# Performance work log

Hardware: AMD Instinct MI355X
Metric: run time of the kernel (lower is better)

## Reference

```python
import jax, jax.numpy as jnp
import numpy as np

N, E = 30000, 480000
HID, NB, D = 256, 128, 2
SW = D * D * NB        # struct-encoder width = bundle_dim^2 * num_bundles = 512
NL, NSAGE = 2, 5       # outer BDL layers, SAGE layers inside struct encoder
OUT = 5
EPS = 1e-5


def _gelu(x):
    return jax.nn.gelu(x, approximate=False)  # torch nn.GELU default (exact)


def _mean_agg(x, src, dst):
    # mean over incoming edges: agg[v] = mean_{u->v} x[u]
    s = jax.ops.segment_sum(x[src], dst, num_segments=N)
    deg = jax.ops.segment_sum(jnp.ones((E,), x.dtype), dst, num_segments=N)
    return s / jnp.maximum(deg, 1.0)[:, None]


def _layernorm(x, g, b):
    m = jnp.mean(x, -1, keepdims=True)
    v = jnp.mean((x - m) ** 2, -1, keepdims=True)
    return (x - m) * jax.lax.rsqrt(v + EPS) * g + b


def _householder(X):
    # torch.nn.utils.parametrizations Orthogonal, orthogonal_map='householder':
    # Q = H_0 H_1 ... H_{d-1}, H_i = I - tau_i v_i v_i^T, v_i = strict-lower col i with unit diag
    d = X.shape[-1]
    A = jnp.tril(X, k=-1)
    tau = 2.0 / (1.0 + jnp.sum(A * A, axis=-2))  # [M, d]
    eye = jnp.eye(d, dtype=X.dtype)
    Q = jnp.broadcast_to(eye, X.shape)
    for i in range(d):
        v = A[:, :, i] + eye[i]
        Qv = jnp.einsum('mij,mj->mi', Q, v)
        Q = Q - tau[:, i, None, None] * Qv[:, :, None] * v[:, None, :]
    return Q


def _struct_encoder(h, src, dst, se_in_w, se_in_b, sage_w1, sage_b1, sage_w2, sage_b2, se_out_w, se_out_b):
    # Model('SAGE', 5, ...) with normalization='None'; dropout inactive in eval
    z = _gelu(h @ se_in_w + se_in_b)
    for i in range(NSAGE):
        m = _mean_agg(z, src, dst)
        zc = jnp.concatenate([z, m], axis=-1)  # SAGE: cat(self, mean(neigh))
        z = z + (_gelu(zc @ sage_w1[i] + sage_b1[i]) @ sage_w2[i] + sage_b2[i])
    return z @ se_out_w + se_out_b


def _forward(x, w_in, b_in, se_in_w, se_in_b, sage_w1, sage_b1, sage_w2, sage_b2,
             se_out_w, se_out_b, enc_w1, enc_b1, enc_w2, enc_b2, ln_g, ln_b,
             bdl_w1, bdl_b1, bdl_w2, bdl_b2, out_ln_g, out_ln_b, w_out, b_out, edge_index):
    src, dst = edge_index[0], edge_index[1]
    h = _gelu(x @ w_in + b_in)
    for k in range(NL):
        enc = _struct_encoder(h, src, dst, se_in_w, se_in_b, sage_w1, sage_b1,
                              sage_w2, sage_b2, se_out_w, se_out_b)
        nr = _gelu(enc @ enc_w1[k] + enc_b1[k]) @ enc_w2[k] + enc_b2[k]  # [N, SW]
        O = _householder(nr.reshape(N * NB, D, D)).reshape(N, NB, D, D)
        # BDL residual module: transport features through per-node bundle frames
        hn = _layernorm(h, ln_g[k], ln_b[k])
        hb = hn.reshape(N, NB, D)
        y = jnp.einsum('nbij,nbj->nbi', O, hb)                       # rotate into frame
        agg = _mean_agg(y.reshape(N, NB * D), src, dst).reshape(N, NB, D)
        msg = jnp.einsum('nbji,nbj->nbi', O, agg).reshape(N, NB * D)  # O^T transports back
        hc = jnp.concatenate([hn, msg], axis=-1)
        h = h + (_gelu(hc @ bdl_w1[k] + bdl_b1[k]) @ bdl_w2[k] + bdl_b2[k])
    h = _layernorm(h, out_ln_g, out_ln_b)
    return h @ w_out + b_out  # [N, OUT]; .squeeze(1) is a no-op for OUT>1


def _w(key, fan_in, shape):
    return jax.random.normal(key, shape, dtype=jnp.float32) / np.sqrt(fan_in)


def setup_inputs() -> dict:
    key = jax.random.key(0)
    ks = iter(jax.random.split(key, 40))
    f32 = jnp.float32
    return {
        'x': jax.random.normal(next(ks), (N, HID), dtype=f32),
        'edge_index': jax.random.randint(next(ks), (2, E), 0, N, dtype=jnp.int32),
        'w_in': _w(next(ks), HID, (HID, HID)), 'b_in': jnp.zeros((HID,), f32),
        'se_in_w': _w(next(ks), HID, (HID, SW)), 'se_in_b': jnp.zeros((SW,), f32),
        'sage_w1': _w(next(ks), 2 * SW, (NSAGE, 2 * SW, SW)), 'sage_b1': jnp.zeros((NSAGE, SW), f32),
        'sage_w2': _w(next(ks), SW, (NSAGE, SW, SW)), 'sage_b2': jnp.zeros((NSAGE, SW), f32),
        'se_out_w': _w(next(ks), SW, (SW, SW)), 'se_out_b': jnp.zeros((SW,), f32),
        'enc_w1': _w(next(ks), SW, (NL, SW, SW)), 'enc_b1': jnp.zeros((NL, SW), f32),
        'enc_w2': _w(next(ks), SW, (NL, SW, SW)), 'enc_b2': jnp.zeros((NL, SW), f32),
        'ln_g': jnp.ones((NL, HID), f32), 'ln_b': jnp.zeros((NL, HID), f32),
        'bdl_w1': _w(next(ks), 2 * HID, (NL, 2 * HID, HID)), 'bdl_b1': jnp.zeros((NL, HID), f32),
        'bdl_w2': _w(next(ks), HID, (NL, HID, HID)), 'bdl_b2': jnp.zeros((NL, HID), f32),
        'out_ln_g': jnp.ones((HID,), f32), 'out_ln_b': jnp.zeros((HID,), f32),
        'w_out': _w(next(ks), HID, (HID, OUT)), 'b_out': jnp.zeros((OUT,), f32),
    }


def reference(x, edge_index, w_in, b_in, se_in_w, se_in_b, sage_w1, sage_b1, sage_w2, sage_b2,
              se_out_w, se_out_b, enc_w1, enc_b1, enc_w2, enc_b2, ln_g, ln_b,
              bdl_w1, bdl_b1, bdl_w2, bdl_b2, out_ln_g, out_ln_b, w_out, b_out):
    return _forward(x, w_in, b_in, se_in_w, se_in_b, sage_w1, sage_b1, sage_w2, sage_b2,
                    se_out_w, se_out_b, enc_w1, enc_b1, enc_w2, enc_b2, ln_g, ln_b,
                    bdl_w1, bdl_b1, bdl_w2, bdl_b2, out_ln_g, out_ln_b, w_out, b_out, edge_index)
```

## Files before the change

kernel.cpp:

```cpp
#include <hip/hip_runtime.h>
#include <hip/hip_bf16.h>
#include <cstdint>
#include <cstddef>


typedef __attribute__((ext_vector_type(8))) short short8;
typedef __attribute__((ext_vector_type(4))) float f32x4;

__device__ __forceinline__ float gelu_exact(float x) {
  return 0.5f * x * (1.0f + erff(x * 0.7071067811865475f));
}
__device__ __forceinline__ unsigned short f2bf(float f) {
  __hip_bfloat16 b = __float2bfloat16(f);
  return *reinterpret_cast<unsigned short*>(&b);
}
__device__ __forceinline__ float bf2f(unsigned short u) {
  return __uint_as_float((unsigned)u << 16);
}
__device__ __forceinline__ float bflo(unsigned u) { return __uint_as_float(u << 16); }
__device__ __forceinline__ float bfhi(unsigned u) { return __uint_as_float(u & 0xffff0000u); }
__device__ __forceinline__ unsigned packbf(float f0, float f1) {
  return (unsigned)f2bf(f0) | ((unsigned)f2bf(f1) << 16);
}
__device__ __forceinline__ void gload16(const void* g, void* l) {
  __builtin_amdgcn_global_load_lds((const __attribute__((address_space(1))) void*)g,
                                   (__attribute__((address_space(3))) void*)l, 16, 0, 0);
}
#define SCHEDB() __builtin_amdgcn_sched_barrier(0)

__global__ void k_hist(const int* __restrict__ dst, int* __restrict__ deg, int E) {
  int i = blockIdx.x * 256 + threadIdx.x;
  if (i < E) atomicAdd(&deg[dst[i]], 1);
}

__global__ __launch_bounds__(1024)
void k_scan(const int* __restrict__ deg, int* __restrict__ rp, int* __restrict__ cur, int Nn) {
  __shared__ int part[1024];
  int t = threadIdx.x;
  int chunk = (Nn + 1023) >> 10;
  int s0 = t * chunk;
  int e0 = s0 + chunk; if (e0 > Nn) e0 = Nn;
  int s = 0;
  for (int i = s0; i < e0; ++i) s += deg[i];
  part[t] = s;
  __syncthreads();
  for (int off = 1; off < 1024; off <<= 1) {
    int v = (t >= off) ? part[t - off] : 0;
    __syncthreads();
    part[t] += v;
    __syncthreads();
  }
  int base = (t == 0) ? 0 : part[t - 1];
  for (int i = s0; i < e0; ++i) {
    rp[i] = base; cur[i] = base; base += deg[i];
  }
  if (t == 0) rp[Nn] = part[1023];
}

__global__ void k_fill(const int* __restrict__ src, const int* __restrict__ dst,
                       int* __restrict__ cur, int* __restrict__ srcs, int E) {
  int i = blockIdx.x * 256 + threadIdx.x;
  if (i < E) {
    int p = atomicAdd(&cur[dst[i]], 1);
    srcs[p] = src[i];
  }
}

__global__ void k_wT(const float* __restrict__ W, unsigned short* __restrict__ Wt, int K, int Nc) {
  const float* Ws = W + (size_t)blockIdx.y * K * Nc;
  unsigned short* Wd = Wt + (size_t)blockIdx.y * K * Nc;
  int idx = blockIdx.x * 256 + threadIdx.x;
  if (idx >= K * Nc) return;
  int k = idx % K, n = idx / K;
  Wd[(size_t)n * K + k] = f2bf(Ws[(size_t)k * Nc + n]);
}

__global__ void k_cast(const float* __restrict__ src, unsigned short* __restrict__ dst, int n) {
  int i = blockIdx.x * 256 + threadIdx.x;
  if (i < n) dst[i] = f2bf(src[i]);
}

template<int ACT, int RES, bool DUAL, bool W32, bool WBF, bool OP>
__global__ __launch_bounds__(256)
void k_mfma(const unsigned short* __restrict__ A1, const unsigned short* __restrict__ A2,
            int K1, int K2,
            const unsigned short* __restrict__ Wt, const float* __restrict__ bias,
            const float* R32, const unsigned short* Rbf,
            float* C32, unsigned short* Cbf, float* Op, int M, int Nc) {
  const int mb_cnt = (M + 127) >> 7;
  const int nb_cnt = Nc >> 7;
  int u = blockIdx.x;
  int xcd = u & 7;
  int rest = u >> 3;
  int nb = rest % nb_cnt;
  int mb = (rest / nb_cnt) * 8 + xcd;
  if (mb >= mb_cnt) return;
  const int m0 = mb << 7, n0 = nb << 7;

  __shared__ unsigned short As[2][128 * 64];
  __shared__ unsigned short Bs[2][128 * 64];
  const int tid = threadIdx.x;
  const int lane = tid & 63, wv = tid >> 6;
  const int wr = (wv >> 1) * 64, wc = (wv & 1) * 64;
  const int rA = lane & 15, kg = lane >> 4;
  const int Ktot = K1 + K2;
  const int nt = Ktot >> 6;

  f32x4 acc[4][4];
#pragma unroll
  for (int m = 0; m < 4; ++m)
#pragma unroll
    for (int n = 0; n < 4; ++n)
#pragma unroll
      for (int r = 0; r < 4; ++r) acc[m][n][r] = 0.f;

  auto stage = [&](int t, int b) {
    int k0 = t << 6;
    const unsigned short* Asrc; int kc, lda;
    if (!DUAL || k0 < K1) { Asrc = A1; kc = k0; lda = K1; }
    else                  { Asrc = A2; kc = k0 - K1; lda = K2; }
#pragma unroll
    for (int is = 0; is < 4; ++is) {
      int chunk = is * 256 + tid;
      int row = chunk >> 3, seg = chunk & 7;
      int ks = seg ^ (row & 7);
      int gm = m0 + row; gm = gm < M ? gm : M - 1;
      gload16(Asrc + (size_t)gm * lda + kc + ks * 8, (char*)As[b] + (size_t)chunk * 16);
      gload16(Wt + (size_t)(n0 + row) * Ktot + k0 + ks * 8, (char*)Bs[b] + (size_t)chunk * 16);
    }
  };

  stage(0, 0);
  if (nt > 1) stage(1, 1);

  for (int t = 0; t < nt; ++t) {
    const int b = t & 1;
    if (t + 1 < nt) asm volatile("s_waitcnt vmcnt(8)" ::: "memory");
    else            asm volatile("s_waitcnt vmcnt(0)" ::: "memory");
    SCHEDB();
    __builtin_amdgcn_s_barrier();
    SCHEDB();

    short8 af[2][4], bq[2][4];
#pragma unroll
    for (int kk = 0; kk < 2; ++kk) {
#pragma unroll
      for (int m = 0; m < 4; ++m) {
        int row = wr + m * 16 + rA;
        int ks = (kk * 4 + kg) ^ (row & 7);
        af[kk][m] = *reinterpret_cast<const short8*>((const char*)As[b] + row * 128 + ks * 16);
      }
#pragma unroll
      for (int n = 0; n < 4; ++n) {
        int col = wc + n * 16 + rA;
        int ks = (kk * 4 + kg) ^ (col & 7);
        bq[kk][n] = *reinterpret_cast<const short8*>((const char*)Bs[b] + col * 128 + ks * 16);
      }
    }
    asm volatile("s_waitcnt lgkmcnt(0)" ::: "memory");
    SCHEDB();
    __builtin_amdgcn_s_barrier();
    SCHEDB();
    if (t + 2 < nt) stage(t + 2, b);

    __builtin_amdgcn_s_setprio(1);
#pragma unroll
    for (int kk = 0; kk < 2; ++kk)
#pragma unroll
      for (int m = 0; m < 4; ++m)
#pragma unroll
        for (int n = 0; n < 4; ++n)
          acc[m][n] = __builtin_amdgcn_mfma_f32_16x16x32_bf16(af[kk][m], bq[kk][n],
                                                              acc[m][n], 0, 0, 0);
    __builtin_amdgcn_s_setprio(0);
  }

#pragma unroll
  for (int m = 0; m < 4; ++m) {
    int gr0 = m0 + wr + m * 16 + kg * 4;
#pragma unroll
    for (int n = 0; n < 4; ++n) {
      int gc = n0 + wc + n * 16 + rA;
      float bv = bias[gc];
#pragma unroll
      for (int r = 0; r < 4; ++r) {
        int gr = gr0 + r;
        if (gr < M) {
          float v = acc[m][n][r] + bv;
          if (ACT == 1) v = gelu_exact(v);
          if (RES == 1) v += R32[(size_t)gr * Nc + gc];
          if (RES == 2) v += bf2f(Rbf[(size_t)gr * Nc + gc]);
          if (W32) C32[(size_t)gr * Nc + gc] = v;
          if (WBF) Cbf[(size_t)gr * Nc + gc] = f2bf(v);
          if (OP) {
            if ((rA & 3) == 2) {
              float iv = 1.0f / (1.0f + v * v);
              float* op = Op + (size_t)gr * 256 + ((gc >> 2) << 1);
              op[0] = (v * v - 1.0f) * iv;
              op[1] = 2.0f * v * iv;
            }
          }
        }
      }
    }
  }
}

template<int W, bool ROT>
__global__ __launch_bounds__(256)
void k_agg(const unsigned short* __restrict__ X, const int* __restrict__ rp,
           const int* __restrict__ srcs, const float* __restrict__ o,
           unsigned short* __restrict__ out, int Nn) {
  int wid = (blockIdx.x * 256 + threadIdx.x) >> 6;
  int lane = threadIdx.x & 63;
  if (wid >= Nn) return;
  constexpr int PE = W / 64;
  float a[PE];
#pragma unroll
  for (int p = 0; p < PE; ++p) a[p] = 0.f;
  int beg = rp[wid], end = rp[wid + 1];
  for (int e = beg; e < end; ++e) {
    int s = srcs[e];
    const unsigned* row = reinterpret_cast<const unsigned*>(X + (size_t)s * W) + lane * (PE / 2);
    if (PE == 8) {
      uint4 v = *reinterpret_cast<const uint4*>(row);
      a[0] += bflo(v.x); a[1] += bfhi(v.x); a[2] += bflo(v.y); a[3] += bfhi(v.y);
      a[4] += bflo(v.z); a[5] += bfhi(v.z); a[6] += bflo(v.w); a[7] += bfhi(v.w);
    } else {
      uint2 v = *reinterpret_cast<const uint2*>(row);
      a[0] += bflo(v.x); a[1] += bfhi(v.x); a[2] += bflo(v.y); a[3] += bfhi(v.y);
    }
  }
  float inv = (end > beg) ? 1.0f / (float)(end - beg) : 0.0f;
#pragma unroll
  for (int p = 0; p < PE; ++p) a[p] *= inv;
  if (ROT) {
    float4 oc = *reinterpret_cast<const float4*>(o + (size_t)wid * 256 + lane * 4);
    float m0 = oc.x * a[0] - oc.y * a[1];
    float m1 = oc.y * a[0] + oc.x * a[1];
    float m2 = oc.z * a[2] - oc.w * a[3];
    float m3 = oc.w * a[2] + oc.z * a[3];
    a[0] = m0; a[1] = m1; a[2] = m2; a[3] = m3;
  }
  unsigned short* op = out + (size_t)wid * W + lane * PE;
  if (PE == 8) {
    uint4 rv;
    rv.x = packbf(a[0], a[1]); rv.y = packbf(a[2], a[3]);
    rv.z = packbf(a[4], a[5]); rv.w = packbf(a[6], a[7]);
    *reinterpret_cast<uint4*>(op) = rv;
  } else {
    uint2 rv;
    rv.x = packbf(a[0], a[1]); rv.y = packbf(a[2], a[3]);
    *reinterpret_cast<uint2*>(op) = rv;
  }
}

__global__ __launch_bounds__(256)
void k_ln_rot(const float* __restrict__ h, const float* __restrict__ o,
              const float* __restrict__ g, const float* __restrict__ b,
              unsigned short* __restrict__ hn, unsigned short* __restrict__ y, int Nn) {
  int wid = (blockIdx.x * 256 + threadIdx.x) >> 6;
  int lane = threadIdx.x & 63;
  if (wid >= Nn) return;
  float4 v = reinterpret_cast<const float4*>(h + (size_t)wid * 256)[lane];
  float s = v.x + v.y + v.z + v.w;
  float ss = v.x * v.x + v.y * v.y + v.z * v.z + v.w * v.w;
#pragma unroll
  for (int off = 1; off < 64; off <<= 1) { s += __shfl_xor(s, off); ss += __shfl_xor(ss, off); }
  float mean = s * (1.0f / 256.0f);
  float var = ss * (1.0f / 256.0f) - mean * mean;
  float rs = rsqrtf(var + 1e-5f);
  float4 gg = reinterpret_cast<const float4*>(g)[lane];
  float4 bb = reinterpret_cast<const float4*>(b)[lane];
  float h0 = (v.x - mean) * rs * gg.x + bb.x;
  float h1 = (v.y - mean) * rs * gg.y + bb.y;
  float h2 = (v.z - mean) * rs * gg.z + bb.z;
  float h3 = (v.w - mean) * rs * gg.w + bb.w;
  uint2 hv; hv.x = packbf(h0, h1); hv.y = packbf(h2, h3);
  *reinterpret_cast<uint2*>(hn + (size_t)wid * 256 + lane * 4) = hv;
  float4 oc = *reinterpret_cast<const float4*>(o + (size_t)wid * 256 + lane * 4);
  float y0 =  oc.x * h0 + oc.y * h1;
  float y1 = -oc.y * h0 + oc.x * h1;
  float y2 =  oc.z * h2 + oc.w * h3;
  float y3 = -oc.w * h2 + oc.z * h3;
  uint2 yv; yv.x = packbf(y0, y1); yv.y = packbf(y2, y3);
  *reinterpret_cast<uint2*>(y + (size_t)wid * 256 + lane * 4) = yv;
}

__global__ __launch_bounds__(256)
void k_final(const float* __restrict__ h, const float* __restrict__ g,
             const float* __restrict__ b, const float* __restrict__ wout,
             const float* __restrict__ bout, float* __restrict__ out, int Nn) {
  int wid = (blockIdx.x * 256 + threadIdx.x) >> 6;
  int lane = threadIdx.x & 63;
  if (wid >= Nn) return;
  float4 v = reinterpret_cast<const float4*>(h + (size_t)wid * 256)[lane];
  float s = v.x + v.y + v.z + v.w;
  float ss = v.x * v.x + v.y * v.y + v.z * v.z + v.w * v.w;
#pragma unroll
  for (int off = 1; off < 64; off <<= 1) { s += __shfl_xor(s, off); ss += __shfl_xor(ss, off); }
  float mean = s * (1.0f / 256.0f);
  float var = ss * (1.0f / 256.0f) - mean * mean;
  float rs = rsqrtf(var + 1e-5f);
  float4 gg = reinterpret_cast<const float4*>(g)[lane];
  float4 bb = reinterpret_cast<const float4*>(b)[lane];
  float hv[4];
  hv[0] = (v.x - mean) * rs * gg.x + bb.x;
  hv[1] = (v.y - mean) * rs * gg.y + bb.y;
  hv[2] = (v.z - mean) * rs * gg.z + bb.z;
  hv[3] = (v.w - mean) * rs * gg.w + bb.w;
  int c0 = lane * 4;
  float dots[5];
#pragma unroll
  for (int j = 0; j < 5; ++j) {
    float p = hv[0] * wout[(size_t)(c0 + 0) * 5 + j] + hv[1] * wout[(size_t)(c0 + 1) * 5 + j]
            + hv[2] * wout[(size_t)(c0 + 2) * 5 + j] + hv[3] * wout[(size_t)(c0 + 3) * 5 + j];
#pragma unroll
    for (int off = 1; off < 64; off <<= 1) p += __shfl_xor(p, off);
    dots[j] = p;
  }
  if (lane == 0) {
#pragma unroll
    for (int j = 0; j < 5; ++j) out[(size_t)wid * 5 + j] = dots[j] + bout[j];
  }
}

extern "C" void kernel_launch(void* const* d_in, const int* in_sizes, int n_in,
                              void* d_out, int out_size, void* d_ws, size_t ws_size,
                              hipStream_t stream) {
  const float* x       = (const float*)d_in[0];
  const int*   ei      = (const int*)  d_in[1];
  const float* w_in    = (const float*)d_in[2];
  const float* b_in    = (const float*)d_in[3];
  const float* se_in_w = (const float*)d_in[4];
  const float* se_in_b = (const float*)d_in[5];
  const float* sage_w1 = (const float*)d_in[6];
  const float* sage_b1 = (const float*)d_in[7];
  const float* sage_w2 = (const float*)d_in[8];
  const float* sage_b2 = (const float*)d_in[9];
  const float* se_out_w= (const float*)d_in[10];
  const float* se_out_b= (const float*)d_in[11];
  const float* enc_w1  = (const float*)d_in[12];
  const float* enc_b1  = (const float*)d_in[13];
  const float* enc_w2  = (const float*)d_in[14];
  const float* enc_b2  = (const float*)d_in[15];
  const float* ln_g    = (const float*)d_in[16];
  const float* ln_b    = (const float*)d_in[17];
  const float* bdl_w1  = (const float*)d_in[18];
  const float* bdl_b1  = (const float*)d_in[19];
  const float* bdl_w2  = (const float*)d_in[20];
  const float* bdl_b2  = (const float*)d_in[21];
  const float* oln_g   = (const float*)d_in[22];
  const float* oln_b   = (const float*)d_in[23];
  const float* w_out   = (const float*)d_in[24];
  const float* b_out   = (const float*)d_in[25];
  float* out = (float*)d_out;

  const int HID = 256, SW = 512;
  const int N = in_sizes[0] / HID;
  const int E = in_sizes[1] / 2;

  float* ws = (float*)d_ws;
  float* h32 = ws;
  float* o   = h32 + (size_t)N * HID;
  unsigned short* h_bf = (unsigned short*)(o + (size_t)N * HID);
  unsigned short* z_bf = h_bf + (size_t)N * HID;
  unsigned short* t_bf = z_bf + (size_t)N * SW;
  unsigned short* u_bf = t_bf + (size_t)N * SW;
  unsigned short* wts = u_bf + (size_t)N * SW;
  size_t off = 0;
  unsigned short* wt_in    = wts + off; off += 256 * 256;
  unsigned short* wt_se_in = wts + off; off += 512 * 256;
  unsigned short* wt_sage1 = wts + off; off += (size_t)5 * 512 * 1024;
  unsigned short* wt_sage2 = wts + off; off += (size_t)5 * 512 * 512;
  unsigned short* wt_se_out= wts + off; off += 512 * 512;
  unsigned short* wt_enc1  = wts + off; off += (size_t)2 * 512 * 512;
  unsigned short* wt_enc2  = wts + off; off += (size_t)2 * 512 * 512;
  unsigned short* wt_bdl1  = wts + off; off += (size_t)2 * 256 * 512;
  unsigned short* wt_bdl2  = wts + off; off += (size_t)2 * 256 * 256;
  int* deg  = (int*)(wts + off);
  int* rp   = deg + N;
  int* cur  = rp + N + 1;
  int* srcs = cur + N;
  size_t need = (size_t)((char*)(srcs + E) - (char*)d_ws);
  if (ws_size < need) return;

  unsigned short* xbf = u_bf;
  unsigned short* hn  = z_bf;
  unsigned short* y   = z_bf + (size_t)N * HID;
  unsigned short* msg = t_bf;
  unsigned short* g2  = u_bf;

  const int* esrc = ei;
  const int* edst = ei + E;

  auto cdiv = [](int a, int b) { return (a + b - 1) / b; };
  dim3 blk(256);
  int mb_cnt = cdiv(N, 128);
  int mgrp = cdiv(mb_cnt, 8);
  int g_g256 = mgrp * 8 * 2;
  int g_g512 = mgrp * 8 * 4;
  int gw = cdiv(N * 64, 256);

  hipMemsetAsync(deg, 0, sizeof(int) * N, stream);
  k_hist<<<cdiv(E, 256), blk, 0, stream>>>(edst, deg, E);
  k_scan<<<1, 1024, 0, stream>>>(deg, rp, cur, N);
  k_fill<<<cdiv(E, 256), blk, 0, stream>>>(esrc, edst, cur, srcs, E);

  auto wT = [&](const float* W, unsigned short* Wt, int K, int Nc, int cnt) {
    k_wT<<<dim3(cdiv(K * Nc, 256), cnt), blk, 0, stream>>>(W, Wt, K, Nc);
  };
  wT(w_in, wt_in, 256, 256, 1);
  wT(se_in_w, wt_se_in, 256, 512, 1);
  wT(sage_w1, wt_sage1, 1024, 512, 5);
  wT(sage_w2, wt_sage2, 512, 512, 5);
  wT(se_out_w, wt_se_out, 512, 512, 1);
  wT(enc_w1, wt_enc1, 512, 512, 2);
  wT(enc_w2, wt_enc2, 512, 512, 2);
  wT(bdl_w1, wt_bdl1, 512, 256, 2);
  wT(bdl_w2, wt_bdl2, 256, 256, 2);
  k_cast<<<cdiv(N * HID, 256), blk, 0, stream>>>(x, xbf, N * HID);

  k_mfma<1, 0, false, true, true, false><<<g_g256, blk, 0, stream>>>(
      xbf, nullptr, 256, 0, wt_in, b_in, nullptr, nullptr, h32, h_bf, nullptr, N, 256);

  for (int k = 0; k < 2; ++k) {
    k_mfma<1, 0, false, false, true, false><<<g_g512, blk, 0, stream>>>(
        h_bf, nullptr, 256, 0, wt_se_in, se_in_b, nullptr, nullptr, nullptr, z_bf, nullptr, N, 512);
    for (int i = 0; i < 5; ++i) {
      k_agg<512, false><<<gw, blk, 0, stream>>>(z_bf, rp, srcs, nullptr, t_bf, N);
      k_mfma<1, 0, true, false, true, false><<<g_g512, blk, 0, stream>>>(
          z_bf, t_bf, 512, 512, wt_sage1 + (size_t)i * 512 * 1024,
          sage_b1 + (size_t)i * SW, nullptr, nullptr, nullptr, u_bf, nullptr, N, 512);
      k_mfma<0, 2, false, false, true, false><<<g_g512, blk, 0, stream>>>(
          u_bf, nullptr, 512, 0, wt_sage2 + (size_t)i * 512 * 512,
          sage_b2 + (size_t)i * SW, nullptr, z_bf, nullptr, z_bf, nullptr, N, 512);
    }
    k_mfma<0, 0, false, false, true, false><<<g_g512, blk, 0, stream>>>(
        z_bf, nullptr, 512, 0, wt_se_out, se_out_b, nullptr, nullptr, nullptr, t_bf, nullptr, N, 512);
    k_mfma<1, 0, false, false, true, false><<<g_g512, blk, 0, stream>>>(
        t_bf, nullptr, 512, 0, wt_enc1 + (size_t)k * 512 * 512,
        enc_b1 + (size_t)k * SW, nullptr, nullptr, nullptr, u_bf, nullptr, N, 512);
    k_mfma<0, 0, false, false, false, true><<<g_g512, blk, 0, stream>>>(
        u_bf, nullptr, 512, 0, wt_enc2 + (size_t)k * 512 * 512,
        enc_b2 + (size_t)k * SW, nullptr, nullptr, nullptr, nullptr, o, N, 512);
    k_ln_rot<<<gw, blk, 0, stream>>>(h32, o, ln_g + (size_t)k * HID, ln_b + (size_t)k * HID, hn, y, N);
    k_agg<256, true><<<gw, blk, 0, stream>>>(y, rp, srcs, o, msg, N);
    k_mfma<1, 0, true, false, true, false><<<g_g256, blk, 0, stream>>>(
        hn, msg, 256, 256, wt_bdl1 + (size_t)k * 256 * 512,
        bdl_b1 + (size_t)k * HID, nullptr, nullptr, nullptr, g2, nullptr, N, 256);
    k_mfma<0, 1, false, true, true, false><<<g_g256, blk, 0, stream>>>(
        g2, nullptr, 256, 0, wt_bdl2 + (size_t)k * 256 * 256,
        bdl_b2 + (size_t)k * HID, h32, nullptr, h32, h_bf, nullptr, N, 256);
  }

  k_final<<<gw, blk, 0, stream>>>(h32, oln_g, oln_b, w_out, b_out, out, N);
}
```

Before: 2.610 ms.

## Fold se_out into enc1 weights and add 256x256-tile MFMA GEMM

Precomputes the product of the struct-encoder output projection and the first encoder weight (plus a fused bias), which removes one N x 512 x 512 GEMM per outer layer. Adds a 512-thread GEMM kernel with 256x256 tiles for all width-512 GEMMs, raising operand reuse per block. Both GEMM kernels now interleave LDS fragment loads with the MFMAs per k-substep. The fused weight is rounded to bf16 after multiplication, which changes numerics slightly, and the larger tile uses more LDS and registers, which may lower occupancy.

```diff
diff --git a/kernel.cpp b/kernel.cpp
--- a/kernel.cpp
+++ b/kernel.cpp
@@ -80,13 +80,24 @@
   if (i < n) dst[i] = f2bf(src[i]);
 }
 
-template<int ACT, int RES, bool DUAL, bool W32, bool WBF, bool OP>
+__global__ void k_bfuse(const float* __restrict__ b_so, const float* __restrict__ W_e1,
+                        const float* __restrict__ b_e1, float* __restrict__ bf) {
+  int k = blockIdx.y;
+  int n = blockIdx.x * 256 + threadIdx.x;
+  if (n >= 512) return;
+  const float* W = W_e1 + (size_t)k * 512 * 512;
+  float s = b_e1[(size_t)k * 512 + n];
+  for (int e = 0; e < 512; ++e) s += b_so[e] * W[(size_t)e * 512 + n];
+  bf[(size_t)k * 512 + n] = s;
+}
+
+template<int ACT, int RES, bool DUAL, bool W32, bool WBF>
 __global__ __launch_bounds__(256)
 void k_mfma(const unsigned short* __restrict__ A1, const unsigned short* __restrict__ A2,
             int K1, int K2,
             const unsigned short* __restrict__ Wt, const float* __restrict__ bias,
             const float* R32, const unsigned short* Rbf,
-            float* C32, unsigned short* Cbf, float* Op, int M, int Nc) {
+            float* C32, unsigned short* Cbf, int M, int Nc) {
   const int mb_cnt = (M + 127) >> 7;
   const int nb_cnt = Nc >> 7;
   int u = blockIdx.x;
@@ -141,38 +152,34 @@
     __builtin_amdgcn_s_barrier();
     SCHEDB();
 
-    short8 af[2][4], bq[2][4];
 #pragma unroll
     for (int kk = 0; kk < 2; ++kk) {
+      short8 bq[4], af[4];
+#pragma unroll
+      for (int n = 0; n < 4; ++n) {
+        int col = wc + n * 16 + rA;
+        int ks = (kk * 4 + kg) ^ (col & 7);
+        bq[n] = *reinterpret_cast<const short8*>((const char*)Bs[b] + col * 128 + ks * 16);
+      }
 #pragma unroll
       for (int m = 0; m < 4; ++m) {
         int row = wr + m * 16 + rA;
         int ks = (kk * 4 + kg) ^ (row & 7);
-        af[kk][m] = *reinterpret_cast<const short8*>((const char*)As[b] + row * 128 + ks * 16);
+        af[m] = *reinterpret_cast<const short8*>((const char*)As[b] + row * 128 + ks * 16);
       }
-#pragma unroll
-      for (int n = 0; n < 4; ++n) {
-        int col = wc + n * 16 + rA;
-        int ks = (kk * 4 + kg) ^ (col & 7);
-        bq[kk][n] = *reinterpret_cast<const short8*>((const char*)Bs[b] + col * 128 + ks * 16);
-      }
+      __builtin_amdgcn_s_setprio(1);
+#pragma unroll
+      for (int m = 0; m < 4; ++m)
+#pragma unroll
+        for (int n = 0; n < 4; ++n)
+          acc[m][n] = __builtin_amdgcn_mfma_f32_16x16x32_bf16(af[m], bq[n], acc[m][n], 0, 0, 0);
+      __builtin_amdgcn_s_setprio(0);
     }
     asm volatile("s_waitcnt lgkmcnt(0)" ::: "memory");
     SCHEDB();
     __builtin_amdgcn_s_barrier();
     SCHEDB();
     if (t + 2 < nt) stage(t + 2, b);
-
-    __builtin_amdgcn_s_setprio(1);
-#pragma unroll
-    for (int kk = 0; kk < 2; ++kk)
-#pragma unroll
-      for (int m = 0; m < 4; ++m)
-#pragma unroll
-        for (int n = 0; n < 4; ++n)
-          acc[m][n] = __builtin_amdgcn_mfma_f32_16x16x32_bf16(af[kk][m], bq[kk][n],
-                                                              acc[m][n], 0, 0, 0);
-    __builtin_amdgcn_s_setprio(0);
   }
 
 #pragma unroll
@@ -187,6 +194,125 @@
         int gr = gr0 + r;
         if (gr < M) {
           float v = acc[m][n][r] + bv;
+          if (ACT == 1) v = gelu_exact(v);
+          if (RES == 1) v += R32[(size_t)gr * Nc + gc];
+          if (RES == 2) v += bf2f(Rbf[(size_t)gr * Nc + gc]);
+          if (W32) C32[(size_t)gr * Nc + gc] = v;
+          if (WBF) Cbf[(size_t)gr * Nc + gc] = f2bf(v);
+        }
+      }
+    }
+  }
+}
+
+template<int ACT, int RES, bool DUAL, bool W32, bool WBF, bool OP>
+__global__ __launch_bounds__(512)
+void k_mfma256(const unsigned short* __restrict__ A1, const unsigned short* __restrict__ A2,
+               int K1, int K2,
+               const unsigned short* __restrict__ Wt, const float* __restrict__ bias,
+               const float* R32, const unsigned short* Rbf,
+               float* C32, unsigned short* Cbf, float* Op, int M, int Nc) {
+  const int mb_cnt = (M + 255) >> 8;
+  const int nb_cnt = Nc >> 8;
+  int u = blockIdx.x;
+  int xcd = u & 7;
+  int rest = u >> 3;
+  int nb = rest % nb_cnt;
+  int mb = (rest / nb_cnt) * 8 + xcd;
+  if (mb >= mb_cnt) return;
+  const int m0 = mb << 8, n0 = nb << 8;
+
+  __shared__ unsigned short As[2][256 * 64];
+  __shared__ unsigned short Bs[2][256 * 64];
+  const int tid = threadIdx.x;
+  const int lane = tid & 63, wv = tid >> 6;
+  const int wm = wv >> 2, wn = wv & 3;
+  const int rA = lane & 15, kg = lane >> 4;
+  const int Ktot = K1 + K2;
+  const int nt = Ktot >> 6;
+
+  f32x4 acc[8][4];
+#pragma unroll
+  for (int f = 0; f < 8; ++f)
+#pragma unroll
+    for (int n = 0; n < 4; ++n)
+#pragma unroll
+      for (int r = 0; r < 4; ++r) acc[f][n][r] = 0.f;
+
+  auto stage = [&](int t, int b) {
+    int k0 = t << 6;
+    const unsigned short* Asrc; int kc, lda;
+    if (!DUAL || k0 < K1) { Asrc = A1; kc = k0; lda = K1; }
+    else                  { Asrc = A2; kc = k0 - K1; lda = K2; }
+#pragma unroll
+    for (int is = 0; is < 4; ++is) {
+      int chunk = is * 512 + tid;
+      int row = chunk >> 3, seg = chunk & 7;
+      int ks = seg ^ (row & 7);
+      int gm = m0 + row; gm = gm < M ? gm : M - 1;
+      gload16(Asrc + (size_t)gm * lda + kc + ks * 8, (char*)As[b] + (size_t)chunk * 16);
+      gload16(Wt + (size_t)(n0 + row) * Ktot + k0 + ks * 8, (char*)Bs[b] + (size_t)chunk * 16);
+    }
+  };
+
+  stage(0, 0);
+  if (nt > 1) stage(1, 1);
+
+  for (int t = 0; t < nt; ++t) {
+    const int b = t & 1;
+    if (t + 1 < nt) asm volatile("s_waitcnt vmcnt(8)" ::: "memory");
+    else            asm volatile("s_waitcnt vmcnt(0)" ::: "memory");
+    SCHEDB();
+    __builtin_amdgcn_s_barrier();
+    SCHEDB();
+
+#pragma unroll
+    for (int kk = 0; kk < 2; ++kk) {
+      short8 bq[4];
+#pragma unroll
+      for (int n = 0; n < 4; ++n) {
+        int col = wn * 64 + n * 16 + rA;
+        int ks = (kk * 4 + kg) ^ (col & 7);
+        bq[n] = *reinterpret_cast<const short8*>((const char*)Bs[b] + col * 128 + ks * 16);
+      }
+#pragma unroll
+      for (int mh = 0; mh < 2; ++mh) {
+        short8 af[4];
+#pragma unroll
+        for (int m = 0; m < 4; ++m) {
+          int row = wm * 128 + (mh * 4 + m) * 16 + rA;
+          int ks = (kk * 4 + kg) ^ (row & 7);
+          af[m] = *reinterpret_cast<const short8*>((const char*)As[b] + row * 128 + ks * 16);
+        }
+        __builtin_amdgcn_s_setprio(1);
+#pragma unroll
+        for (int m = 0; m < 4; ++m)
+#pragma unroll
+          for (int n = 0; n < 4; ++n)
+            acc[mh * 4 + m][n] =
+                __builtin_amdgcn_mfma_f32_16x16x32_bf16(af[m], bq[n], acc[mh * 4 + m][n], 0, 0, 0);
+        __builtin_amdgcn_s_setprio(0);
+      }
+    }
+    asm volatile("s_waitcnt lgkmcnt(0)" ::: "memory");
+    SCHEDB();
+    __builtin_amdgcn_s_barrier();
+    SCHEDB();
+    if (t + 2 < nt) stage(t + 2, b);
+  }
+
+#pragma unroll
+  for (int f = 0; f < 8; ++f) {
+    int gr0 = m0 + wm * 128 + f * 16 + kg * 4;
+#pragma unroll
+    for (int n = 0; n < 4; ++n) {
+      int gc = n0 + wn * 64 + n * 16 + rA;
+      float bv = bias[gc];
+#pragma unroll
+      for (int r = 0; r < 4; ++r) {
+        int gr = gr0 + r;
+        if (gr < M) {
+          float v = acc[f][n][r] + bv;
           if (ACT == 1) v = gelu_exact(v);
           if (RES == 1) v += R32[(size_t)gr * Nc + gc];
           if (RES == 2) v += bf2f(Rbf[(size_t)gr * Nc + gc]);
@@ -373,11 +499,14 @@
   unsigned short* wt_se_in = wts + off; off += 512 * 256;
   unsigned short* wt_sage1 = wts + off; off += (size_t)5 * 512 * 1024;
   unsigned short* wt_sage2 = wts + off; off += (size_t)5 * 512 * 512;
-  unsigned short* wt_se_out= wts + off; off += 512 * 512;
+  unsigned short* so_bf    = wts + off; off += 512 * 512;
   unsigned short* wt_enc1  = wts + off; off += (size_t)2 * 512 * 512;
   unsigned short* wt_enc2  = wts + off; off += (size_t)2 * 512 * 512;
   unsigned short* wt_bdl1  = wts + off; off += (size_t)2 * 256 * 512;
   unsigned short* wt_bdl2  = wts + off; off += (size_t)2 * 256 * 256;
+  unsigned short* wt_f     = wts + off; off += (size_t)2 * 512 * 512;
+  float* bf_f = (float*)(wts + off); off += 2 * 512 * 2;
+  float* zb   = (float*)(wts + off); off += 512 * 2;
   int* deg  = (int*)(wts + off);
   int* rp   = deg + N;
   int* cur  = rp + N + 1;
@@ -396,10 +525,12 @@
 
   auto cdiv = [](int a, int b) { return (a + b - 1) / b; };
   dim3 blk(256);
-  int mb_cnt = cdiv(N, 128);
-  int mgrp = cdiv(mb_cnt, 8);
-  int g_g256 = mgrp * 8 * 2;
-  int g_g512 = mgrp * 8 * 4;
+  dim3 blk512(512);
+  int mb128 = cdiv(N, 128), mg128 = cdiv(mb128, 8);
+  int g128_n256 = mg128 * 8 * 2;
+  int mb256 = cdiv(N, 256), mg256 = cdiv(mb256, 8);
+  int g256_n512 = mg256 * 8 * 2;
+  int gF = 1 * 8 * 2;
   int gw = cdiv(N * 64, 256);
 
   hipMemsetAsync(deg, 0, sizeof(int) * N, stream);
@@ -414,44 +545,48 @@
   wT(se_in_w, wt_se_in, 256, 512, 1);
   wT(sage_w1, wt_sage1, 1024, 512, 5);
   wT(sage_w2, wt_sage2, 512, 512, 5);
-  wT(se_out_w, wt_se_out, 512, 512, 1);
   wT(enc_w1, wt_enc1, 512, 512, 2);
   wT(enc_w2, wt_enc2, 512, 512, 2);
   wT(bdl_w1, wt_bdl1, 512, 256, 2);
   wT(bdl_w2, wt_bdl2, 256, 256, 2);
+  k_cast<<<cdiv(512 * 512, 256), blk, 0, stream>>>(se_out_w, so_bf, 512 * 512);
   k_cast<<<cdiv(N * HID, 256), blk, 0, stream>>>(x, xbf, N * HID);
-
-  k_mfma<1, 0, false, true, true, false><<<g_g256, blk, 0, stream>>>(
-      xbf, nullptr, 256, 0, wt_in, b_in, nullptr, nullptr, h32, h_bf, nullptr, N, 256);
+  hipMemsetAsync(zb, 0, 512 * sizeof(float), stream);
+  k_bfuse<<<dim3(2, 2), blk, 0, stream>>>(se_out_b, enc_w1, enc_b1, bf_f);
+  for (int k = 0; k < 2; ++k)
+    k_mfma256<0, 0, false, false, true, false><<<gF, blk512, 0, stream>>>(
+        wt_enc1 + (size_t)k * 512 * 512, nullptr, 512, 0, so_bf, zb,
+        nullptr, nullptr, nullptr, wt_f + (size_t)k * 512 * 512, nullptr, 512, 512);
+
+  k_mfma<1, 0, false, true, true><<<g128_n256, blk, 0, stream>>>(
+      xbf, nullptr, 256, 0, wt_in, b_in, nullptr, nullptr, h32, h_bf, N, 256);
 
   for (int k = 0; k < 2; ++k) {
-    k_mfma<1, 0, false, false, true, false><<<g_g512, blk, 0, stream>>>(
+    k_mfma256<1, 0, false, false, true, false><<<g256_n512, blk512, 0, stream>>>(
         h_bf, nullptr, 256, 0, wt_se_in, se_in_b, nullptr, nullptr, nullptr, z_bf, nullptr, N, 512);
     for (int i = 0; i < 5; ++i) {
       k_agg<512, false><<<gw, blk, 0, stream>>>(z_bf, rp, srcs, nullptr, t_bf, N);
-      k_mfma<1, 0, true, false, true, false><<<g_g512, blk, 0, stream>>>(
+      k_mfma256<1, 0, true, false, true, false><<<g256_n512, blk512, 0, stream>>>(
           z_bf, t_bf, 512, 512, wt_sage1 + (size_t)i * 512 * 1024,
           sage_b1 + (size_t)i * SW, nullptr, nullptr, nullptr, u_bf, nullptr, N, 512);
-      k_mfma<0, 2, false, false, true, false><<<g_g512, blk, 0, stream>>>(
+      k_mfma256<0, 2, false, false, true, false><<<g256_n512, blk512, 0, stream>>>(
           u_bf, nullptr, 512, 0, wt_sage2 + (size_t)i * 512 * 512,
           sage_b2 + (size_t)i * SW, nullptr, z_bf, nullptr, z_bf, nullptr, N, 512);
     }
-    k_mfma<0, 0, false, false, true, false><<<g_g512, blk, 0, stream>>>(
-        z_bf, nullptr, 512, 0, wt_se_out, se_out_b, nullptr, nullptr, nullptr, t_bf, nullptr, N, 512);
-    k_mfma<1, 0, false, false, true, false><<<g_g512, blk, 0, stream>>>(
-        t_bf, nullptr, 512, 0, wt_enc1 + (size_t)k * 512 * 512,
-        enc_b1 + (size_t)k * SW, nullptr, nullptr, nullptr, u_bf, nullptr, N, 512);
-    k_mfma<0, 0, false, false, false, true><<<g_g512, blk, 0, stream>>>(
+    k_mfma256<1, 0, false, false, true, false><<<g256_n512, blk512, 0, stream>>>(
+        z_bf, nullptr, 512, 0, wt_f + (size_t)k * 512 * 512,
+        bf_f + (size_t)k * 512, nullptr, nullptr, nullptr, u_bf, nullptr, N, 512);
+    k_mfma256<0, 0, false, false, false, true><<<g256_n512, blk512, 0, stream>>>(
         u_bf, nullptr, 512, 0, wt_enc2 + (size_t)k * 512 * 512,
         enc_b2 + (size_t)k * SW, nullptr, nullptr, nullptr, nullptr, o, N, 512);
     k_ln_rot<<<gw, blk, 0, stream>>>(h32, o, ln_g + (size_t)k * HID, ln_b + (size_t)k * HID, hn, y, N);
     k_agg<256, true><<<gw, blk, 0, stream>>>(y, rp, srcs, o, msg, N);
-    k_mfma<1, 0, true, false, true, false><<<g_g256, blk, 0, stream>>>(
+    k_mfma<1, 0, true, false, true><<<g128_n256, blk, 0, stream>>>(
         hn, msg, 256, 256, wt_bdl1 + (size_t)k * 256 * 512,
-        bdl_b1 + (size_t)k * HID, nullptr, nullptr, nullptr, g2, nullptr, N, 256);
-    k_mfma<0, 1, false, true, true, false><<<g_g256, blk, 0, stream>>>(
+        bdl_b1 + (size_t)k * HID, nullptr, nullptr, nullptr, g2, N, 256);
+    k_mfma<0, 1, false, true, true><<<g128_n256, blk, 0, stream>>>(
         g2, nullptr, 256, 0, wt_bdl2 + (size_t)k * 256 * 256,
-        bdl_b2 + (size_t)k * HID, h32, nullptr, h32, h_bf, nullptr, N, 256);
+        bdl_b2 + (size_t)k * HID, h32, nullptr, h32, h_bf, N, 256);
   }
 
   k_final<<<gw, blk, 0, stream>>>(h32, oln_g, oln_b, w_out, b_out, out, N);
```

After: 2.666 ms. +2.1%, slower.
